# Performance work log

Hardware: AMD Instinct MI355X
Metric: run time of the kernel (lower is better)

## Reference

```python
import jax, jax.numpy as jnp
import numpy as np

B, N, L, S, H, E, D = 4, 32, 256, 256, 8, 64, 64

def setup_inputs() -> dict:
    key = jax.random.key(0)
    k1, k2, k3, k4 = jax.random.split(key, 4)
    queries = jax.random.normal(k1, (B, N, L, H, E), dtype=jnp.float32)
    keys = jax.random.normal(k2, (B, N, S, H, E), dtype=jnp.float32)
    values = jax.random.normal(k3, (B, N, S, H, D), dtype=jnp.float32)
    # additive causal mask [L, S]: 0 where allowed, -1e9 where masked
    causal = jnp.tril(jnp.ones((L, S), dtype=bool))
    attn_mask = jnp.where(causal, 0.0, -1e9).astype(jnp.float32)
    # cross-layer accumulated prior scores [B, N, H, L, S]
    attn_scores = jax.random.normal(k4, (B, N, H, L, S), dtype=jnp.float32) * 0.1
    query_lengths = jnp.full((B,), L, dtype=jnp.int32)
    key_lengths = jnp.full((B,), S, dtype=jnp.int32)
    return {"queries": queries, "keys": keys, "values": values,
            "attn_mask": attn_mask, "attn_scores": attn_scores,
            "query_lengths": query_lengths, "key_lengths": key_lengths}

def reference(queries, keys, values, attn_mask, attn_scores, query_lengths, key_lengths):
    # queries: [B,N,L,H,E], keys: [B,N,S,H,E], values: [B,N,S,H,D]
    e = queries.shape[-1]
    softmax_temp = 1.0 / np.sqrt(e).astype(np.float32)
    QK = jnp.einsum('bnlhe,bnshe->bnhls', queries, keys)
    # additive mask broadcast over [B,N,H]
    scores = QK + attn_mask + attn_scores  # accumulated scores returned for next layer
    A = jax.nn.softmax(softmax_temp * scores, axis=-1)  # dropout omitted (eval mode)
    V = jnp.einsum('bnhls,bnshd->bnlhd', A, values)
    return scores, V
```

## Files before the change

### kernel.cpp

```cpp
#include <hip/hip_runtime.h>
#include <stdint.h>


typedef __attribute__((ext_vector_type(8))) short bfrag;
typedef __attribute__((ext_vector_type(4))) float f32x4;
typedef __attribute__((ext_vector_type(2))) float f32x2;
typedef __attribute__((ext_vector_type(4))) int i32x4;

__device__ __forceinline__ uint32_t f2bf(float f) {
  uint32_t u = __builtin_bit_cast(uint32_t, f);
  return (u + 0x7FFFu + ((u >> 16) & 1u)) >> 16;
}
__device__ __forceinline__ uint32_t pk(float a, float b) {
  return f2bf(a) | (f2bf(b) << 16);
}

#define MFMA(a, b, c) __builtin_amdgcn_mfma_f32_16x16x32_bf16((a), (b), (c), 0, 0, 0)

__global__ __launch_bounds__(1024, 2) void attn_kernel(
    const float* __restrict__ Qg, const float* __restrict__ Kg,
    const float* __restrict__ Vg, const float* __restrict__ Pg,
    float* __restrict__ Sc, float* __restrict__ Ov)
{
  __shared__ char Kb[2][4096];
  __shared__ char Vb[2][4096];

  const int t = threadIdx.x;
  const int lane = t & 63;
  const int wave = t >> 6;
  const int ql = lane & 15;
  const int g  = lane >> 4;
  const int qt = (int)((0x783C96D25A1EB4F0ull >> (wave * 4)) & 15);
  const int q = qt * 16 + ql;
  const int pvmax = qt >> 1;
  const int swzk = (ql & 7) << 4;
  const int swzv = (ql & 3) << 4;
  const float temp = 0.125f;

  const int kr_ = t >> 5;
  const int kc_ = t & 31;
  const int vd_ = t & 63;
  const int vw_ = t >> 6;
  const int kwoff = (kr_ * 128 + kc_ * 4) ^ ((kr_ & 7) << 4);
  const int vwoff = (vd_ * 64 + vw_ * 4) ^ ((vd_ & 3) << 4);

#pragma unroll 1
  for (int bi = 0; bi < 4; ++bi) {
    const int bnh = (bi << 8) + blockIdx.x;
    const int bn = bnh >> 3, h = bnh & 7;

    const float* kgp = Kg + (size_t)bn * 131072 + h * 64 + (size_t)kr_ * 512 + 2 * kc_;
    const float* vgp = Vg + (size_t)bn * 131072 + h * 64 + (size_t)(2 * vw_) * 512 + vd_;

    f32x2 kreg = *(const f32x2*)kgp;
    float vreg0 = vgp[0], vreg1 = vgp[512];
    *(uint32_t*)(&Kb[0][0] + kwoff) = pk(kreg[0], kreg[1]);
    *(uint32_t*)(&Vb[0][0] + vwoff) = pk(vreg0, vreg1);
    kreg = *(const f32x2*)(kgp + 16384);
    vreg0 = vgp[16384];
    vreg1 = vgp[16384 + 512];

    bfrag qf[2];
#pragma unroll
    for (int ks = 0; ks < 2; ++ks) {
      const float* qp = Qg + (size_t)bn * 131072 + (size_t)q * 512 + h * 64 + ks * 32 + g * 8;
      const f32x4 qa = *(const f32x4*)qp;
      const f32x4 qb = *(const f32x4*)(qp + 4);
      union { i32x4 i; bfrag b; } u;
      u.i = i32x4{(int)pk(qa.x, qa.y), (int)pk(qa.z, qa.w),
                  (int)pk(qb.x, qb.y), (int)pk(qb.z, qb.w)};
      qf[ks] = u.b;
    }

    f32x4 O[4];
#pragma unroll
    for (int ds = 0; ds < 4; ++ds) O[ds] = f32x4{0.f, 0.f, 0.f, 0.f};
    float m = -1e30f, lsum = 0.f;

    const size_t scb = (size_t)bnh << 16;
    const float* prp = Pg + scb + (size_t)q * 256 + 4 * g;
    float* scp = Sc + scb + (size_t)q * 256 + 4 * g;

    f32x4 pr0 = __builtin_nontemporal_load((const f32x4*)(prp));
    f32x4 pr1 = __builtin_nontemporal_load((const f32x4*)(prp + 16));

    asm volatile("s_waitcnt lgkmcnt(0)" ::: "memory");
    __builtin_amdgcn_s_barrier();

#pragma unroll 1
    for (int st = 0; st < 8; ++st) {
      const int s0 = st * 32;
      const int p = (st & 1) << 12;
      bfrag kf[2][2];
#pragma unroll
      for (int ss = 0; ss < 2; ++ss)
#pragma unroll
        for (int ks = 0; ks < 2; ++ks)
          kf[ss][ks] = *(const bfrag*)(&Kb[0][0] + p +
              (((16 * ss + ql) * 128 + ks * 64 + g * 16) ^ swzk));

      f32x4 acc[2];
#pragma unroll
      for (int ss = 0; ss < 2; ++ss) {
        f32x4 a = f32x4{0.f, 0.f, 0.f, 0.f};
        a = MFMA(kf[ss][0], qf[0], a);
        a = MFMA(kf[ss][1], qf[1], a);
        const int sb = s0 + 16 * ss + 4 * g;
#pragma unroll
        for (int r = 0; r < 4; ++r)
          a[r] = (sb + r <= q) ? a[r] : a[r] - 1e9f;
        acc[ss] = a + (ss == 0 ? pr0 : pr1);
      }

      if (st < 7) {
        pr0 = __builtin_nontemporal_load((const f32x4*)(prp + (st + 1) * 32));
        pr1 = __builtin_nontemporal_load((const f32x4*)(prp + (st + 1) * 32 + 16));
      }

      __builtin_nontemporal_store(acc[0], (f32x4*)(scp + s0));
      __builtin_nontemporal_store(acc[1], (f32x4*)(scp + s0 + 16));

      if (st <= pvmax) {
        float tm = fmaxf(fmaxf(fmaxf(acc[0][0], acc[0][1]), fmaxf(acc[0][2], acc[0][3])),
                         fmaxf(fmaxf(acc[1][0], acc[1][1]), fmaxf(acc[1][2], acc[1][3])));
        tm = fmaxf(tm, __shfl_xor(tm, 16));
        tm = fmaxf(tm, __shfl_xor(tm, 32));
        tm *= temp;
        const float mnew = fmaxf(m, tm);
        const float fct = __expf(m - mnew);
        m = mnew;
        float pv[8];
#pragma unroll
        for (int ss = 0; ss < 2; ++ss)
#pragma unroll
          for (int r = 0; r < 4; ++r)
            pv[ss * 4 + r] = __expf(fmaf(temp, acc[ss][r], -mnew));
        float ts = (pv[0] + pv[1]) + (pv[2] + pv[3]) + (pv[4] + pv[5]) + (pv[6] + pv[7]);
        ts += __shfl_xor(ts, 16);
        ts += __shfl_xor(ts, 32);
        lsum = lsum * fct + ts;
#pragma unroll
        for (int ds = 0; ds < 4; ++ds) O[ds] *= fct;

        const int w0x = (int)pk(pv[0], pv[1]), w0y = (int)pk(pv[2], pv[3]);
        const int w1x = (int)pk(pv[4], pv[5]), w1y = (int)pk(pv[6], pv[7]);
        const int srcA = ((g & 1) << 5) + ql;
        const int a0 = __shfl(w0x, srcA),      a1 = __shfl(w1x, srcA);
        const int b0 = __shfl(w0y, srcA),      b1 = __shfl(w1y, srcA);
        const int c0 = __shfl(w0x, srcA + 16), c1 = __shfl(w1x, srcA + 16);
        const int d0 = __shfl(w0y, srcA + 16), d1 = __shfl(w1y, srcA + 16);
        union { i32x4 i; bfrag b; } pu;
        pu.i = i32x4{g < 2 ? a0 : a1, g < 2 ? b0 : b1,
                     g < 2 ? c0 : c1, g < 2 ? d0 : d1};

        bfrag vf[4];
#pragma unroll
        for (int ds = 0; ds < 4; ++ds)
          vf[ds] = *(const bfrag*)(&Vb[0][0] + p +
              (((16 * ds + ql) * 64 + g * 16) ^ swzv));
#pragma unroll
        for (int ds = 0; ds < 4; ++ds) O[ds] = MFMA(vf[ds], pu.b, O[ds]);
      }

      if (st < 7) {
        const int p1 = ((st + 1) & 1) << 12;
        *(uint32_t*)(&Kb[0][0] + p1 + kwoff) = pk(kreg[0], kreg[1]);
        *(uint32_t*)(&Vb[0][0] + p1 + vwoff) = pk(vreg0, vreg1);
        if (st < 6) {
          kreg = *(const f32x2*)(kgp + (size_t)(st + 2) * 16384);
          vreg0 = vgp[(st + 2) * 16384];
          vreg1 = vgp[(st + 2) * 16384 + 512];
        }
      }
      asm volatile("s_waitcnt lgkmcnt(0)" ::: "memory");
      __builtin_amdgcn_s_barrier();
    }

    {
      const float inv = 1.f / lsum;
      float* op = Ov + (size_t)bn * 131072 + (size_t)q * 512 + h * 64 + 4 * g;
#pragma unroll
      for (int ds = 0; ds < 4; ++ds) {
        f32x4 o = O[ds] * inv;
        *(f32x4*)(op + 16 * ds) = o;
      }
    }
  }
}

extern "C" void kernel_launch(void* const* d_in, const int* in_sizes, int n_in,
                              void* d_out, int out_size, void* d_ws, size_t ws_size,
                              hipStream_t stream) {
  const float* Qg = (const float*)d_in[0];
  const float* Kg = (const float*)d_in[1];
  const float* Vg = (const float*)d_in[2];
  const float* Pg = (const float*)d_in[4];
  float* Sc = (float*)d_out;
  float* Ov = Sc + (size_t)4 * 32 * 8 * 256 * 256;
  attn_kernel<<<dim3(256), dim3(1024), 0, stream>>>(Qg, Kg, Vg, Pg, Sc, Ov);
}
```

Baseline: 150.6 us.

## Unroll tile loop by two and prefetch prior scores two tiles ahead

The per-tile loop is manually unrolled by two with a macro, so each half uses a compile-time LDS buffer offset and its own register pair for the prior-score tile. This lets the prior-score loads be issued two tiles ahead instead of one, giving more time to hide the global-memory latency of the largest input stream. Launch bounds are relaxed from 2 to 1 block per CU, giving the compiler more registers per thread. With 1024-thread blocks and a 256-block grid, occupancy may not change much in practice.

```diff
diff --git a/kernel.cpp b/kernel.cpp
--- a/kernel.cpp
+++ b/kernel.cpp
@@ -17,7 +17,7 @@
 
 #define MFMA(a, b, c) __builtin_amdgcn_mfma_f32_16x16x32_bf16((a), (b), (c), 0, 0, 0)
 
-__global__ __launch_bounds__(1024, 2) void attn_kernel(
+__global__ __launch_bounds__(1024, 1) void attn_kernel(
     const float* __restrict__ Qg, const float* __restrict__ Kg,
     const float* __restrict__ Vg, const float* __restrict__ Pg,
     float* __restrict__ Sc, float* __restrict__ Ov)
@@ -81,100 +81,94 @@
     const float* prp = Pg + scb + (size_t)q * 256 + 4 * g;
     float* scp = Sc + scb + (size_t)q * 256 + 4 * g;
 
-    f32x4 pr0 = __builtin_nontemporal_load((const f32x4*)(prp));
-    f32x4 pr1 = __builtin_nontemporal_load((const f32x4*)(prp + 16));
+    f32x4 prA0 = __builtin_nontemporal_load((const f32x4*)(prp));
+    f32x4 prA1 = __builtin_nontemporal_load((const f32x4*)(prp + 16));
+    f32x4 prB0 = __builtin_nontemporal_load((const f32x4*)(prp + 32));
+    f32x4 prB1 = __builtin_nontemporal_load((const f32x4*)(prp + 48));
 
     asm volatile("s_waitcnt lgkmcnt(0)" ::: "memory");
     __builtin_amdgcn_s_barrier();
 
+#define TILE_BODY(ST, PR0, PR1, PLIT)                                          \
+    {                                                                          \
+      const int s0 = (ST) * 32;                                                \
+      bfrag kf[2][2];                                                          \
+      _Pragma("unroll") for (int ss = 0; ss < 2; ++ss)                         \
+          _Pragma("unroll") for (int ks = 0; ks < 2; ++ks)                     \
+              kf[ss][ks] = *(const bfrag*)(&Kb[0][0] + (PLIT) +                \
+                  (((16 * ss + ql) * 128 + ks * 64 + g * 16) ^ swzk));         \
+      f32x4 acc[2];                                                            \
+      _Pragma("unroll") for (int ss = 0; ss < 2; ++ss) {                       \
+        f32x4 a = f32x4{0.f, 0.f, 0.f, 0.f};                                   \
+        a = MFMA(kf[ss][0], qf[0], a);                                         \
+        a = MFMA(kf[ss][1], qf[1], a);                                         \
+        const int sb = s0 + 16 * ss + 4 * g;                                   \
+        _Pragma("unroll") for (int r = 0; r < 4; ++r)                          \
+            a[r] = (sb + r <= q) ? a[r] : a[r] - 1e9f;                         \
+        acc[ss] = a + (ss == 0 ? PR0 : PR1);                                   \
+      }                                                                        \
+      if ((ST) + 2 < 8) {           \
+        PR0 = __builtin_nontemporal_load((const f32x4*)(prp + ((ST) + 2) * 32)); \
+        PR1 = __builtin_nontemporal_load((const f32x4*)(prp + ((ST) + 2) * 32 + 16)); \
+      }                                                                        \
+      __builtin_nontemporal_store(acc[0], (f32x4*)(scp + s0));                 \
+      __builtin_nontemporal_store(acc[1], (f32x4*)(scp + s0 + 16));            \
+      if ((ST) <= pvmax) {                                                     \
+        float tm = fmaxf(fmaxf(fmaxf(acc[0][0], acc[0][1]), fmaxf(acc[0][2], acc[0][3])), \
+                         fmaxf(fmaxf(acc[1][0], acc[1][1]), fmaxf(acc[1][2], acc[1][3]))); \
+        tm = fmaxf(tm, __shfl_xor(tm, 16));                                    \
+        tm = fmaxf(tm, __shfl_xor(tm, 32));                                    \
+        tm *= temp;                                                            \
+        const float mnew = fmaxf(m, tm);                                       \
+        const float fct = __expf(m - mnew);                                    \
+        m = mnew;                                                              \
+        float pv[8];                                                           \
+        _Pragma("unroll") for (int ss = 0; ss < 2; ++ss)                       \
+            _Pragma("unroll") for (int r = 0; r < 4; ++r)                      \
+                pv[ss * 4 + r] = __expf(fmaf(temp, acc[ss][r], -mnew));        \
+        float ts = (pv[0] + pv[1]) + (pv[2] + pv[3]) + (pv[4] + pv[5]) + (pv[6] + pv[7]); \
+        ts += __shfl_xor(ts, 16);                                              \
+        ts += __shfl_xor(ts, 32);                                              \
+        lsum = lsum * fct + ts;                                                \
+        _Pragma("unroll") for (int ds = 0; ds < 4; ++ds) O[ds] *= fct;         \
+        const int w0x = (int)pk(pv[0], pv[1]), w0y = (int)pk(pv[2], pv[3]);    \
+        const int w1x = (int)pk(pv[4], pv[5]), w1y = (int)pk(pv[6], pv[7]);    \
+        const int srcA = ((g & 1) << 5) + ql;                                  \
+        const int a0 = __shfl(w0x, srcA),      a1 = __shfl(w1x, srcA);         \
+        const int b0 = __shfl(w0y, srcA),      b1 = __shfl(w1y, srcA);         \
+        const int c0 = __shfl(w0x, srcA + 16), c1 = __shfl(w1x, srcA + 16);    \
+        const int d0 = __shfl(w0y, srcA + 16), d1 = __shfl(w1y, srcA + 16);    \
+        union { i32x4 i; bfrag b; } pu;                                        \
+        pu.i = i32x4{g < 2 ? a0 : a1, g < 2 ? b0 : b1,                         \
+                     g < 2 ? c0 : c1, g < 2 ? d0 : d1};                        \
+        bfrag vf[4];                                                           \
+        _Pragma("unroll") for (int ds = 0; ds < 4; ++ds)                       \
+            vf[ds] = *(const bfrag*)(&Vb[0][0] + (PLIT) +                      \
+                (((16 * ds + ql) * 64 + g * 16) ^ swzv));                      \
+        _Pragma("unroll") for (int ds = 0; ds < 4; ++ds)                       \
+            O[ds] = MFMA(vf[ds], pu.b, O[ds]);                                 \
+      }                                                                        \
+      if ((ST) < 7) {     \
+        *(uint32_t*)(&Kb[0][0] + ((PLIT) ^ 4096) + kwoff) = pk(kreg[0], kreg[1]); \
+        *(uint32_t*)(&Vb[0][0] + ((PLIT) ^ 4096) + vwoff) = pk(vreg0, vreg1);  \
+        if ((ST) < 6) {                                                        \
+          kreg = *(const f32x2*)(kgp + (size_t)((ST) + 2) * 16384);            \
+          vreg0 = vgp[((ST) + 2) * 16384];                                     \
+          vreg1 = vgp[((ST) + 2) * 16384 + 512];                               \
+        }                                                                      \
+      }                                                                        \
+      asm volatile("s_waitcnt lgkmcnt(0)" ::: "memory");                       \
+      __builtin_amdgcn_s_barrier();                                            \
+    }
+
 #pragma unroll 1
-    for (int st = 0; st < 8; ++st) {
-      const int s0 = st * 32;
-      const int p = (st & 1) << 12;
-      bfrag kf[2][2];
-#pragma unroll
-      for (int ss = 0; ss < 2; ++ss)
-#pragma unroll
-        for (int ks = 0; ks < 2; ++ks)
-          kf[ss][ks] = *(const bfrag*)(&Kb[0][0] + p +
-              (((16 * ss + ql) * 128 + ks * 64 + g * 16) ^ swzk));
-
-      f32x4 acc[2];
-#pragma unroll
-      for (int ss = 0; ss < 2; ++ss) {
-        f32x4 a = f32x4{0.f, 0.f, 0.f, 0.f};
-        a = MFMA(kf[ss][0], qf[0], a);
-        a = MFMA(kf[ss][1], qf[1], a);
-        const int sb = s0 + 16 * ss + 4 * g;
-#pragma unroll
-        for (int r = 0; r < 4; ++r)
-          a[r] = (sb + r <= q) ? a[r] : a[r] - 1e9f;
-        acc[ss] = a + (ss == 0 ? pr0 : pr1);
-      }
-
-      if (st < 7) {
-        pr0 = __builtin_nontemporal_load((const f32x4*)(prp + (st + 1) * 32));
-        pr1 = __builtin_nontemporal_load((const f32x4*)(prp + (st + 1) * 32 + 16));
-      }
-
-      __builtin_nontemporal_store(acc[0], (f32x4*)(scp + s0));
-      __builtin_nontemporal_store(acc[1], (f32x4*)(scp + s0 + 16));
-
-      if (st <= pvmax) {
-        float tm = fmaxf(fmaxf(fmaxf(acc[0][0], acc[0][1]), fmaxf(acc[0][2], acc[0][3])),
-                         fmaxf(fmaxf(acc[1][0], acc[1][1]), fmaxf(acc[1][2], acc[1][3])));
-        tm = fmaxf(tm, __shfl_xor(tm, 16));
-        tm = fmaxf(tm, __shfl_xor(tm, 32));
-        tm *= temp;
-        const float mnew = fmaxf(m, tm);
-        const float fct = __expf(m - mnew);
-        m = mnew;
-        float pv[8];
-#pragma unroll
-        for (int ss = 0; ss < 2; ++ss)
-#pragma unroll
-          for (int r = 0; r < 4; ++r)
-            pv[ss * 4 + r] = __expf(fmaf(temp, acc[ss][r], -mnew));
-        float ts = (pv[0] + pv[1]) + (pv[2] + pv[3]) + (pv[4] + pv[5]) + (pv[6] + pv[7]);
-        ts += __shfl_xor(ts, 16);
-        ts += __shfl_xor(ts, 32);
-        lsum = lsum * fct + ts;
-#pragma unroll
-        for (int ds = 0; ds < 4; ++ds) O[ds] *= fct;
-
-        const int w0x = (int)pk(pv[0], pv[1]), w0y = (int)pk(pv[2], pv[3]);
-        const int w1x = (int)pk(pv[4], pv[5]), w1y = (int)pk(pv[6], pv[7]);
-        const int srcA = ((g & 1) << 5) + ql;
-        const int a0 = __shfl(w0x, srcA),      a1 = __shfl(w1x, srcA);
-        const int b0 = __shfl(w0y, srcA),      b1 = __shfl(w1y, srcA);
-        const int c0 = __shfl(w0x, srcA + 16), c1 = __shfl(w1x, srcA + 16);
-        const int d0 = __shfl(w0y, srcA + 16), d1 = __shfl(w1y, srcA + 16);
-        union { i32x4 i; bfrag b; } pu;
-        pu.i = i32x4{g < 2 ? a0 : a1, g < 2 ? b0 : b1,
-                     g < 2 ? c0 : c1, g < 2 ? d0 : d1};
-
-        bfrag vf[4];
-#pragma unroll
-        for (int ds = 0; ds < 4; ++ds)
-          vf[ds] = *(const bfrag*)(&Vb[0][0] + p +
-              (((16 * ds + ql) * 64 + g * 16) ^ swzv));
-#pragma unroll
-        for (int ds = 0; ds < 4; ++ds) O[ds] = MFMA(vf[ds], pu.b, O[ds]);
-      }
-
-      if (st < 7) {
-        const int p1 = ((st + 1) & 1) << 12;
-        *(uint32_t*)(&Kb[0][0] + p1 + kwoff) = pk(kreg[0], kreg[1]);
-        *(uint32_t*)(&Vb[0][0] + p1 + vwoff) = pk(vreg0, vreg1);
-        if (st < 6) {
-          kreg = *(const f32x2*)(kgp + (size_t)(st + 2) * 16384);
-          vreg0 = vgp[(st + 2) * 16384];
-          vreg1 = vgp[(st + 2) * 16384 + 512];
-        }
-      }
-      asm volatile("s_waitcnt lgkmcnt(0)" ::: "memory");
-      __builtin_amdgcn_s_barrier();
+    for (int tt = 0; tt < 4; ++tt) {
+      const int stE = tt * 2;
+      TILE_BODY(stE, prA0, prA1, 0)
+      const int stO = tt * 2 + 1;
+      TILE_BODY(stO, prB0, prB1, 4096)
     }
+#undef TILE_BODY
 
     {
       const float inv = 1.f / lsum;
```

Measured after the change: 156.6 us. +4.0%, slower.
